# Performance work log

Hardware: AMD Instinct MI355X
Metric: run time of the kernel (lower is better)

The kernel has to match this reference:

```python
import jax, jax.numpy as jnp
import numpy as np

B, S, D = 8, 2048, 2048
E, R, K = 8, 16, 2
NUM_TASKS, NUM_MODES = 4, 2
ALPHA = 16.0


def setup_inputs() -> dict:
    key = jax.random.key(0)
    k1, k2, k3, k4 = jax.random.split(key, 4)
    hidden_states = jax.random.normal(k1, (B, S, D), dtype=jnp.float32)
    gate_w = jax.random.normal(k2, (E, D), dtype=jnp.float32) * 0.01  # nn.init.normal_(std=0.01)
    # Soft-prior biases: fill(-1.0), strong prior 3.0 / 2.0 at configured (task, expert) / (mode, expert)
    tb = -np.ones((NUM_TASKS, E), dtype=np.float32)
    mb = -np.ones((NUM_MODES, E), dtype=np.float32)
    for e in range(E):
        tb[e % NUM_TASKS, e] = 3.0
        mb[e % NUM_MODES, e] = 2.0
    # LoRA params; lora_B is zero-init in torch but we use small random values for a nontrivial baseline
    lora_A = jax.random.normal(k3, (E, R, D), dtype=jnp.float32) * (1.0 / np.sqrt(D))
    lora_B = jax.random.normal(k4, (E, D, R), dtype=jnp.float32) * 0.02
    return {
        "hidden_states": hidden_states,
        "gate_w": gate_w,
        "task_bias": jnp.asarray(tb),
        "mode_bias": jnp.asarray(mb),
        "lora_A": lora_A,
        "lora_B": lora_B,
        "task_id": 1,
        "mode_id": 1,
    }


def reference(hidden_states, gate_w, task_bias, mode_bias, lora_A, lora_B, task_id, mode_id):
    scaling = ALPHA / R
    # Router: score = dynamic_gate(mean_pool(x)) + task_bias[t] + mode_bias[m]
    x_pooled = hidden_states.mean(axis=1)                       # [B, D]
    logits = x_pooled @ gate_w.T + task_bias[task_id] + mode_bias[mode_id]  # [B, E]
    top_v, top_i = jax.lax.top_k(logits, K)                     # [B, K]
    weights = jax.nn.softmax(top_v, axis=-1)                    # [B, K]
    # per-sample, per-expert combine weight: sum of top-k weights routed to that expert
    one_hot = jax.nn.one_hot(top_i, E, dtype=weights.dtype)     # [B, K, E]
    sw = jnp.einsum('bke,bk->be', one_hot, weights)             # [B, E]
    # LoRA experts: (x @ A_e^T) @ B_e^T * scaling, weighted-summed per sample
    mid = jnp.einsum('bsd,erd->besr', hidden_states, lora_A)    # [B, E, S, R] (small: R=16)
    out = jnp.einsum('be,besr,edr->bsd', sw, mid, lora_B) * scaling  # [B, S, D]
    return out
```

## Files before the change

### kernel.cpp

```cpp
#include <hip/hip_runtime.h>
#include <stdint.h>

typedef __attribute__((ext_vector_type(8))) short bf16x8;
typedef __attribute__((ext_vector_type(4))) float f32x4;
typedef unsigned short ushort_t;

#define B_ 8
#define S_ 2048
#define D_ 2048
#define E_ 8
#define J_ 128

static __device__ __forceinline__ unsigned short f2bf(float f) {
  union { float f; uint32_t u; } v; v.f = f;
  uint32_t u = v.u;
  return (unsigned short)((u + 0x7FFFu + ((u >> 16) & 1u)) >> 16);
}
static __device__ __forceinline__ float bf2f(ushort_t h) {
  union { uint32_t u; float f; } v; v.u = ((uint32_t)h) << 16;
  return v.f;
}

#define GLL16(gsrc, ldst)                                                        \
  __builtin_amdgcn_global_load_lds(                                              \
      (const __attribute__((address_space(1))) void*)(gsrc),                     \
      (__attribute__((address_space(3))) void*)(ldst), 16, 0, 0)

#define VMBAR(N)                                                                 \
  asm volatile("s_waitcnt vmcnt(" #N ") lgkmcnt(0)\n\ts_barrier" ::: "memory")

__global__ void k_prep(const float* __restrict__ lA, const float* __restrict__ lB,
                       ushort_t* __restrict__ Ag, ushort_t* __restrict__ Bg) {
  int gid = blockIdx.x * blockDim.x + threadIdx.x;
  int stride = gridDim.x * blockDim.x;
  for (int o = gid; o < 32 * 128 * 8 * 8; o += stride) {
    int wi = o & 7, ch = o >> 3;
    int kt = ch >> 10, i = ch & 1023;
    int j = i >> 3, c = i & 7;
    int d = kt * 64 + (((c ^ j) & 7) << 3) + wi;
    Ag[o] = f2bf(lA[j * D_ + d]);
  }
  for (int o4 = gid; o4 < (D_ * J_) / 4; o4 += stride) {
    int j4 = o4 & 31, dd = o4 >> 5;
    int e = j4 >> 2, r0 = (j4 & 3) * 4;
    float4 v = *(const float4*)(lB + ((size_t)e * D_ + dd) * 16 + r0);
    uint2 pk;
    pk.x = (uint32_t)f2bf(v.x) | ((uint32_t)f2bf(v.y) << 16);
    pk.y = (uint32_t)f2bf(v.z) | ((uint32_t)f2bf(v.w) << 16);
    ((uint2*)Bg)[o4] = pk;
  }
}

__global__ __launch_bounds__(256) void k_mid(const float* __restrict__ x,
    const ushort_t* __restrict__ Ag, const float* __restrict__ gw,
    ushort_t* __restrict__ midb, float* __restrict__ lpart) {
  __shared__ float Xs[3][2048];
  __shared__ ushort_t Ab[2][8192];
  __shared__ float poolL[2048];
  __shared__ float tmpP[2][4][64];
  const int tid = threadIdx.x;
  const int w = tid >> 6, lane = tid & 63;
  const int lm = lane & 15, g = lane >> 4;
  const int b = blockIdx.y, s0 = blockIdx.x * 32;
  const int row16 = (w & 1) * 16, jbase = (w >> 1) * 64;
  const float* xb = x + ((size_t)(b * S_ + s0)) * D_;

  f32x4 acc[4] = {};

  auto stageX = [&](int buf, int kt) {
    const int d0 = kt * 64;
#pragma unroll
    for (int c = 0; c < 2; ++c) {
      int i = c * 256 + w * 64 + lane;
      int row = i >> 4, ch = i & 15;
      const float* src = xb + (size_t)row * D_ + d0 + ((ch ^ (row & 7)) << 2);
      GLL16(src, &Xs[buf][(c * 256 + w * 64) * 4]);
    }
  };
  auto stageA = [&](int buf, int kt) {
#pragma unroll
    for (int c = 0; c < 4; ++c) {
      const ushort_t* src = Ag + (size_t)kt * 8192 + (size_t)(c * 256 + w * 64 + lane) * 8;
      GLL16(src, &Ab[buf][(c * 256 + w * 64) * 8]);
    }
  };
  auto computeTile = [&](int t, int xcb, int acb) {
    const int r = row16 + lm;
#pragma unroll
    for (int ks = 0; ks < 2; ++ks) {
      const int c0 = ks * 8 + g * 2;
      float4 v0 = *(const float4*)&Xs[xcb][r * 64 + ((c0 ^ (r & 7)) << 2)];
      float4 v1 = *(const float4*)&Xs[xcb][r * 64 + (((c0 + 1) ^ (r & 7)) << 2)];
      bf16x8 xf;
      xf[0] = (short)f2bf(v0.x); xf[1] = (short)f2bf(v0.y);
      xf[2] = (short)f2bf(v0.z); xf[3] = (short)f2bf(v0.w);
      xf[4] = (short)f2bf(v1.x); xf[5] = (short)f2bf(v1.y);
      xf[6] = (short)f2bf(v1.z); xf[7] = (short)f2bf(v1.w);
#pragma unroll
      for (int nn = 0; nn < 4; ++nn) {
        int jr = jbase + nn * 16 + lm;
        bf16x8 af = *(const bf16x8*)&Ab[acb][jr * 64 + (((ks * 4 + g) ^ (jr & 7)) << 3)];
        acc[nn] = __builtin_amdgcn_mfma_f32_16x16x32_bf16(af, xf, acc[nn], 0, 0, 0);
      }
    }
    float s = 0.f;
#pragma unroll
    for (int i = 0; i < 8; ++i) {
      int rr = w * 8 + i;
      s += Xs[xcb][rr * 64 + (((lane >> 2) ^ (rr & 7)) << 2) + (lane & 3)];
    }
    tmpP[t & 1][w][lane] = s;
  };
  auto foldTile = [&](int tau) {
    if (w == (tau & 3)) {
      float cs = tmpP[tau & 1][0][lane] + tmpP[tau & 1][1][lane] +
                 tmpP[tau & 1][2][lane] + tmpP[tau & 1][3][lane];
      poolL[tau * 64 + lane] = cs;
    }
  };

  stageA(0, 0);
  __builtin_amdgcn_sched_barrier(0);
  stageX(0, 0);
  __builtin_amdgcn_sched_barrier(0);
  stageX(1, 1);
  __builtin_amdgcn_sched_barrier(0);

  int xcb = 0, xsb = 2;
  for (int t = 0; t < 31; ++t) {
    VMBAR(2);
    __builtin_amdgcn_sched_barrier(0);
    const int acb = t & 1;
    stageA(acb ^ 1, t + 1);
    __builtin_amdgcn_sched_barrier(0);
    if (t + 2 < 32) stageX(xsb, t + 2);
    __builtin_amdgcn_sched_barrier(0);
    if (t > 0) foldTile(t - 1);
    computeTile(t, xcb, acb);
    xcb = (xcb == 2) ? 0 : xcb + 1;
    xsb = (xsb == 2) ? 0 : xsb + 1;
  }
  VMBAR(0);
  __builtin_amdgcn_sched_barrier(0);
  foldTile(30);
  computeTile(31, xcb, 1);

  ushort_t* mp = midb + ((size_t)(b * S_ + s0 + row16 + lm)) * J_ + jbase;
#pragma unroll
  for (int nn = 0; nn < 4; ++nn) {
    uint2 pk;
    pk.x = (uint32_t)f2bf(acc[nn][0]) | ((uint32_t)f2bf(acc[nn][1]) << 16);
    pk.y = (uint32_t)f2bf(acc[nn][2]) | ((uint32_t)f2bf(acc[nn][3]) << 16);
    *(uint2*)&mp[nn * 16 + g * 4] = pk;
  }

  __syncthreads();
  foldTile(31);
  __syncthreads();

  float lp[8] = {0.f, 0.f, 0.f, 0.f, 0.f, 0.f, 0.f, 0.f};
#pragma unroll
  for (int k = 0; k < 8; ++k) {
    float pv = poolL[k * 256 + tid];
#pragma unroll
    for (int e = 0; e < 8; ++e) lp[e] += pv * gw[(size_t)e * D_ + k * 256 + tid];
  }
#pragma unroll
  for (int e = 0; e < 8; ++e) {
    float v = lp[e];
    v += __shfl_xor(v, 32); v += __shfl_xor(v, 16); v += __shfl_xor(v, 8);
    v += __shfl_xor(v, 4);  v += __shfl_xor(v, 2);  v += __shfl_xor(v, 1);
    if (lane == 0) tmpP[0][w][e] = v;
  }
  __syncthreads();
  if (tid < 8) {
    float s = tmpP[0][0][tid] + tmpP[0][1][tid] + tmpP[0][2][tid] + tmpP[0][3][tid];
    lpart[((size_t)(b * 64 + blockIdx.x)) * 8 + tid] = s;
  }
}

__global__ void k_router(const float* __restrict__ lpart,
                         const float* __restrict__ tb, const float* __restrict__ mb,
                         const int* __restrict__ task_p, const int* __restrict__ mode_p,
                         float* __restrict__ rinfo) {
  __shared__ float lg[64];
  const int t = threadIdx.x;
  const int b = t >> 3, e = t & 7;
  float s = 0.f;
  for (int k = 0; k < 64; ++k) s += lpart[((size_t)(b * 64 + k)) * 8 + e];
  lg[t] = s * (1.f / (float)S_) + tb[task_p[0] * E_ + e] + mb[mode_p[0] * E_ + e];
  __syncthreads();
  if (t < B_) {
    float v[8];
#pragma unroll
    for (int e2 = 0; e2 < 8; ++e2) v[e2] = lg[t * 8 + e2];
    int i1 = 0;
#pragma unroll
    for (int e2 = 1; e2 < 8; ++e2) if (v[e2] > v[i1]) i1 = e2;
    int i2 = (i1 == 0) ? 1 : 0;
#pragma unroll
    for (int e2 = 0; e2 < 8; ++e2) if (e2 != i1 && v[e2] > v[i2]) i2 = e2;
    float ex = __expf(v[i2] - v[i1]);
    float w1 = 1.f / (1.f + ex), w2 = ex * w1;
    float4 r;
    r.x = (float)i1; r.y = (float)i2; r.z = w1; r.w = w2;
    ((float4*)rinfo)[t] = r;
  }
}

__global__ __launch_bounds__(256) void k_comb(const ushort_t* __restrict__ midb,
    const float* __restrict__ rinfo, const ushort_t* __restrict__ Bg,
    float* __restrict__ out) {
  __shared__ ushort_t Bt[128][40];
  const int n = blockIdx.x, m = blockIdx.y, b = blockIdx.z;
  const int tid = threadIdx.x, w = tid >> 6, lane = tid & 63;
  const int lm = lane & 15, g = lane >> 4;

  const float4 ri = ((const float4*)rinfo)[b];
  const int i1 = (int)ri.x, i2 = (int)ri.y;
  const float w1 = ri.z, w2 = ri.w;

#pragma unroll
  for (int c = 0; c < 2; ++c) {
    int ci = c * 256 + tid;
    int d = ci >> 2, sub = ci & 3;
    int e = (sub & 2) ? i2 : i1;
    float sc = (sub & 2) ? w2 : w1;
    bf16x8 bv = *(const bf16x8*)(Bg + ((size_t)(n * 128 + d)) * J_ + e * 16 + (sub & 1) * 8);
    bf16x8 bw;
#pragma unroll
    for (int i = 0; i < 8; ++i) bw[i] = (short)f2bf(bf2f((ushort_t)bv[i]) * sc);
    *(bf16x8*)&Bt[d][sub * 8] = bw;
  }

  const int srow = m * 64 + w * 16 + lm;
  const int jw = (g < 2) ? (i1 * 16 + g * 8) : (i2 * 16 + (g - 2) * 8);
  bf16x8 pf = *(const bf16x8*)&midb[((size_t)(b * S_ + srow)) * J_ + jw];
  __syncthreads();

  f32x4 acc[8] = {};
#pragma unroll
  for (int nn = 0; nn < 8; ++nn) {
    bf16x8 af = *(const bf16x8*)&Bt[nn * 16 + lm][g * 8];
    acc[nn] = __builtin_amdgcn_mfma_f32_16x16x32_bf16(af, pf, acc[nn], 0, 0, 0);
  }

  float* op = out + ((size_t)(b * S_ + srow)) * D_ + n * 128;
#pragma unroll
  for (int nn = 0; nn < 8; ++nn)
    *(f32x4*)&op[nn * 16 + g * 4] = acc[nn];
}

extern "C" void kernel_launch(void* const* d_in, const int* in_sizes, int n_in,
                              void* d_out, int out_size, void* d_ws, size_t ws_size,
                              hipStream_t stream) {
  const float* x    = (const float*)d_in[0];
  const float* gw   = (const float*)d_in[1];
  const float* tb   = (const float*)d_in[2];
  const float* mb   = (const float*)d_in[3];
  const float* lA   = (const float*)d_in[4];
  const float* lB   = (const float*)d_in[5];
  const int* task_p = (const int*)d_in[6];
  const int* mode_p = (const int*)d_in[7];
  float* out = (float*)d_out;
  char* ws = (char*)d_ws;
  ushort_t* midb  = (ushort_t*)ws;
  ushort_t* Ag    = (ushort_t*)(ws + 4194304);
  ushort_t* Bg    = (ushort_t*)(ws + 4718592);
  float* lpart    = (float*)(ws + 5242880);
  float* rinfo    = (float*)(ws + 5259264);

  hipLaunchKernelGGL(k_prep, dim3(256), dim3(256), 0, stream, lA, lB, Ag, Bg);
  hipLaunchKernelGGL(k_mid, dim3(64, 8), dim3(256), 0, stream, x, Ag, gw, midb, lpart);
  hipLaunchKernelGGL(k_router, dim3(1), dim3(64), 0, stream,
                     lpart, tb, mb, task_p, mode_p, rinfo);
  hipLaunchKernelGGL(k_comb, dim3(16, 32, 8), dim3(256), 0, stream, midb, rinfo, Bg, out);
}
```

Baseline: 88.78 us.

## Fold router gate into LoRA-A MFMA and load x directly into registers

The gate weights are appended as extra rows (padded to 160) to the bf16 LoRA-A tile, so the router logits come out of the same MFMA pass as mid instead of a separate mean-pool and fp32 gate dot product in the kernel tail. The x tile is now read from global memory straight into registers with double buffering instead of being staged through LDS, which frees shared memory and removes the LDS pooling reductions. The gate projection is now done with bf16 x and gate weights rather than fp32, which can perturb logits and top-k routing. Wave 3 also does extra MFMA work, so the waves are unbalanced.

```diff
diff --git a/kernel.cpp b/kernel.cpp
--- a/kernel.cpp
+++ b/kernel.cpp
@@ -10,6 +10,8 @@
 #define D_ 2048
 #define E_ 8
 #define J_ 128
+#define AROWS 160
+#define ATILE (AROWS * 64)
 
 static __device__ __forceinline__ unsigned short f2bf(float f) {
   union { float f; uint32_t u; } v; v.f = f;
@@ -27,18 +29,30 @@
       (__attribute__((address_space(3))) void*)(ldst), 16, 0, 0)
 
 #define VMBAR(N)                                                                 \
-  asm volatile("s_waitcnt vmcnt(" #N ") lgkmcnt(0)\n\ts_barrier" ::: "memory")
+  asm volatile("s_waitcnt vmcnt(" #N ")\n\ts_barrier" ::: "memory")
 
 __global__ void k_prep(const float* __restrict__ lA, const float* __restrict__ lB,
-                       ushort_t* __restrict__ Ag, ushort_t* __restrict__ Bg) {
+                       const float* __restrict__ gw,
+                       ushort_t* __restrict__ AgE, ushort_t* __restrict__ Bg) {
   int gid = blockIdx.x * blockDim.x + threadIdx.x;
   int stride = gridDim.x * blockDim.x;
-  for (int o = gid; o < 32 * 128 * 8 * 8; o += stride) {
-    int wi = o & 7, ch = o >> 3;
-    int kt = ch >> 10, i = ch & 1023;
-    int j = i >> 3, c = i & 7;
-    int d = kt * 64 + (((c ^ j) & 7) << 3) + wi;
-    Ag[o] = f2bf(lA[j * D_ + d]);
+  for (int o = gid; o < 32 * AROWS * 8; o += stride) {
+    int kt = o / (AROWS * 8);
+    int rem = o - kt * (AROWS * 8);
+    int row = rem >> 3, c = rem & 7;
+    int d = kt * 64 + (((c ^ row) & 7) << 3);
+    bf16x8 outv = {};
+    if (row < 136) {
+      const float* src = (row < 128) ? (lA + (size_t)row * D_ + d)
+                                     : (gw + (size_t)(row - 128) * D_ + d);
+      float4 v0 = *(const float4*)src;
+      float4 v1 = *(const float4*)(src + 4);
+      outv[0] = (short)f2bf(v0.x); outv[1] = (short)f2bf(v0.y);
+      outv[2] = (short)f2bf(v0.z); outv[3] = (short)f2bf(v0.w);
+      outv[4] = (short)f2bf(v1.x); outv[5] = (short)f2bf(v1.y);
+      outv[6] = (short)f2bf(v1.z); outv[7] = (short)f2bf(v1.w);
+    }
+    *(bf16x8*)&AgE[(size_t)o * 8] = outv;
   }
   for (int o4 = gid; o4 < (D_ * J_) / 4; o4 += stride) {
     int j4 = o4 & 31, dd = o4 >> 5;
@@ -52,130 +66,123 @@
 }
 
 __global__ __launch_bounds__(256) void k_mid(const float* __restrict__ x,
-    const ushort_t* __restrict__ Ag, const float* __restrict__ gw,
-    ushort_t* __restrict__ midb, float* __restrict__ lpart) {
-  __shared__ float Xs[3][2048];
-  __shared__ ushort_t Ab[2][8192];
-  __shared__ float poolL[2048];
-  __shared__ float tmpP[2][4][64];
+    const ushort_t* __restrict__ AgE, ushort_t* __restrict__ midb,
+    float* __restrict__ lpart) {
+  __shared__ ushort_t Ab[2][ATILE];
   const int tid = threadIdx.x;
   const int w = tid >> 6, lane = tid & 63;
   const int lm = lane & 15, g = lane >> 4;
   const int b = blockIdx.y, s0 = blockIdx.x * 32;
-  const int row16 = (w & 1) * 16, jbase = (w >> 1) * 64;
-  const float* xb = x + ((size_t)(b * S_ + s0)) * D_;
-
-  f32x4 acc[4] = {};
-
-  auto stageX = [&](int buf, int kt) {
-    const int d0 = kt * 64;
-#pragma unroll
-    for (int c = 0; c < 2; ++c) {
-      int i = c * 256 + w * 64 + lane;
-      int row = i >> 4, ch = i & 15;
-      const float* src = xb + (size_t)row * D_ + d0 + ((ch ^ (row & 7)) << 2);
-      GLL16(src, &Xs[buf][(c * 256 + w * 64) * 4]);
-    }
-  };
+  const int tn0 = w, tn1 = w + 4;
+  const float* xrow = x + ((size_t)(b * S_ + s0 + lm)) * D_ + g * 8;
+
+  f32x4 acc0[2] = {}, acc1[2] = {}, acc2[2] = {};
+
   auto stageA = [&](int buf, int kt) {
 #pragma unroll
-    for (int c = 0; c < 4; ++c) {
-      const ushort_t* src = Ag + (size_t)kt * 8192 + (size_t)(c * 256 + w * 64 + lane) * 8;
-      GLL16(src, &Ab[buf][(c * 256 + w * 64) * 8]);
-    }
-  };
-  auto computeTile = [&](int t, int xcb, int acb) {
-    const int r = row16 + lm;
+    for (int c = 0; c < 5; ++c) {
+      int ch = c * 256 + tid;
+      const ushort_t* src = AgE + (size_t)kt * ATILE + (size_t)ch * 8;
+      GLL16(src, &Ab[buf][ch * 8]);
+    }
+  };
+  auto loadX = [&](float4* xr, int t) {
+    const float* p0 = xrow + t * 64;
+    const float* p1 = p0 + 16 * D_;
+    xr[0] = *(const float4*)(p0);
+    xr[1] = *(const float4*)(p0 + 4);
+    xr[2] = *(const float4*)(p0 + 32);
+    xr[3] = *(const float4*)(p0 + 36);
+    xr[4] = *(const float4*)(p1);
+    xr[5] = *(const float4*)(p1 + 4);
+    xr[6] = *(const float4*)(p1 + 32);
+    xr[7] = *(const float4*)(p1 + 36);
+  };
+  auto computeTile = [&](int t, const float4* xr) {
+    const ushort_t* Ac = &Ab[t & 1][0];
+    bf16x8 xf[2][2];
+#pragma unroll
+    for (int sh = 0; sh < 2; ++sh)
+#pragma unroll
+      for (int ks = 0; ks < 2; ++ks) {
+        float4 v0 = xr[sh * 4 + ks * 2];
+        float4 v1 = xr[sh * 4 + ks * 2 + 1];
+        bf16x8 f;
+        f[0] = (short)f2bf(v0.x); f[1] = (short)f2bf(v0.y);
+        f[2] = (short)f2bf(v0.z); f[3] = (short)f2bf(v0.w);
+        f[4] = (short)f2bf(v1.x); f[5] = (short)f2bf(v1.y);
+        f[6] = (short)f2bf(v1.z); f[7] = (short)f2bf(v1.w);
+        xf[sh][ks] = f;
+      }
 #pragma unroll
     for (int ks = 0; ks < 2; ++ks) {
-      const int c0 = ks * 8 + g * 2;
-      float4 v0 = *(const float4*)&Xs[xcb][r * 64 + ((c0 ^ (r & 7)) << 2)];
-      float4 v1 = *(const float4*)&Xs[xcb][r * 64 + (((c0 + 1) ^ (r & 7)) << 2)];
-      bf16x8 xf;
-      xf[0] = (short)f2bf(v0.x); xf[1] = (short)f2bf(v0.y);
-      xf[2] = (short)f2bf(v0.z); xf[3] = (short)f2bf(v0.w);
-      xf[4] = (short)f2bf(v1.x); xf[5] = (short)f2bf(v1.y);
-      xf[6] = (short)f2bf(v1.z); xf[7] = (short)f2bf(v1.w);
-#pragma unroll
-      for (int nn = 0; nn < 4; ++nn) {
-        int jr = jbase + nn * 16 + lm;
-        bf16x8 af = *(const bf16x8*)&Ab[acb][jr * 64 + (((ks * 4 + g) ^ (jr & 7)) << 3)];
-        acc[nn] = __builtin_amdgcn_mfma_f32_16x16x32_bf16(af, xf, acc[nn], 0, 0, 0);
+      const int chs = (((ks * 4 + g) ^ (lm & 7)) << 3);
+      bf16x8 a0 = *(const bf16x8*)&Ac[(tn0 * 16 + lm) * 64 + chs];
+      bf16x8 a1 = *(const bf16x8*)&Ac[(tn1 * 16 + lm) * 64 + chs];
+#pragma unroll
+      for (int sh = 0; sh < 2; ++sh) {
+        acc0[sh] = __builtin_amdgcn_mfma_f32_16x16x32_bf16(a0, xf[sh][ks], acc0[sh], 0, 0, 0);
+        acc1[sh] = __builtin_amdgcn_mfma_f32_16x16x32_bf16(a1, xf[sh][ks], acc1[sh], 0, 0, 0);
       }
-    }
-    float s = 0.f;
-#pragma unroll
-    for (int i = 0; i < 8; ++i) {
-      int rr = w * 8 + i;
-      s += Xs[xcb][rr * 64 + (((lane >> 2) ^ (rr & 7)) << 2) + (lane & 3)];
-    }
-    tmpP[t & 1][w][lane] = s;
-  };
-  auto foldTile = [&](int tau) {
-    if (w == (tau & 3)) {
-      float cs = tmpP[tau & 1][0][lane] + tmpP[tau & 1][1][lane] +
-                 tmpP[tau & 1][2][lane] + tmpP[tau & 1][3][lane];
-      poolL[tau * 64 + lane] = cs;
-    }
-  };
-
+      if (w == 3) {
+        bf16x8 a2 = *(const bf16x8*)&Ac[(128 + lm) * 64 + chs];
+#pragma unroll
+        for (int sh = 0; sh < 2; ++sh)
+          acc2[sh] = __builtin_amdgcn_mfma_f32_16x16x32_bf16(a2, xf[sh][ks], acc2[sh], 0, 0, 0);
+      }
+    }
+  };
+
+  float4 xA[8], xB[8];
   stageA(0, 0);
   __builtin_amdgcn_sched_barrier(0);
-  stageX(0, 0);
+  loadX(xA, 0);
   __builtin_amdgcn_sched_barrier(0);
-  stageX(1, 1);
+
+  auto body = [&](int t, const float4* xc, float4* xn) {
+    VMBAR(8);
+    __builtin_amdgcn_sched_barrier(0);
+    stageA((t + 1) & 1, t + 1);
+    __builtin_amdgcn_sched_barrier(0);
+    loadX(xn, t + 1);
+    __builtin_amdgcn_sched_barrier(0);
+    computeTile(t, xc);
+  };
+
+  for (int tt = 0; tt < 15; ++tt) {
+    body(2 * tt, xA, xB);
+    body(2 * tt + 1, xB, xA);
+  }
+  body(30, xA, xB);
+  VMBAR(8);
   __builtin_amdgcn_sched_barrier(0);
-
-  int xcb = 0, xsb = 2;
-  for (int t = 0; t < 31; ++t) {
-    VMBAR(2);
-    __builtin_amdgcn_sched_barrier(0);
-    const int acb = t & 1;
-    stageA(acb ^ 1, t + 1);
-    __builtin_amdgcn_sched_barrier(0);
-    if (t + 2 < 32) stageX(xsb, t + 2);
-    __builtin_amdgcn_sched_barrier(0);
-    if (t > 0) foldTile(t - 1);
-    computeTile(t, xcb, acb);
-    xcb = (xcb == 2) ? 0 : xcb + 1;
-    xsb = (xsb == 2) ? 0 : xsb + 1;
-  }
-  VMBAR(0);
-  __builtin_amdgcn_sched_barrier(0);
-  foldTile(30);
-  computeTile(31, xcb, 1);
-
-  ushort_t* mp = midb + ((size_t)(b * S_ + s0 + row16 + lm)) * J_ + jbase;
-#pragma unroll
-  for (int nn = 0; nn < 4; ++nn) {
-    uint2 pk;
-    pk.x = (uint32_t)f2bf(acc[nn][0]) | ((uint32_t)f2bf(acc[nn][1]) << 16);
-    pk.y = (uint32_t)f2bf(acc[nn][2]) | ((uint32_t)f2bf(acc[nn][3]) << 16);
-    *(uint2*)&mp[nn * 16 + g * 4] = pk;
-  }
-
-  __syncthreads();
-  foldTile(31);
-  __syncthreads();
-
-  float lp[8] = {0.f, 0.f, 0.f, 0.f, 0.f, 0.f, 0.f, 0.f};
-#pragma unroll
-  for (int k = 0; k < 8; ++k) {
-    float pv = poolL[k * 256 + tid];
-#pragma unroll
-    for (int e = 0; e < 8; ++e) lp[e] += pv * gw[(size_t)e * D_ + k * 256 + tid];
-  }
-#pragma unroll
-  for (int e = 0; e < 8; ++e) {
-    float v = lp[e];
-    v += __shfl_xor(v, 32); v += __shfl_xor(v, 16); v += __shfl_xor(v, 8);
-    v += __shfl_xor(v, 4);  v += __shfl_xor(v, 2);  v += __shfl_xor(v, 1);
-    if (lane == 0) tmpP[0][w][e] = v;
-  }
-  __syncthreads();
-  if (tid < 8) {
-    float s = tmpP[0][0][tid] + tmpP[0][1][tid] + tmpP[0][2][tid] + tmpP[0][3][tid];
-    lpart[((size_t)(b * 64 + blockIdx.x)) * 8 + tid] = s;
+  computeTile(31, xB);
+
+#pragma unroll
+  for (int sh = 0; sh < 2; ++sh) {
+    ushort_t* mp = midb + ((size_t)(b * S_ + s0 + sh * 16 + lm)) * J_;
+    uint2 pk0, pk1;
+    pk0.x = (uint32_t)f2bf(acc0[sh][0]) | ((uint32_t)f2bf(acc0[sh][1]) << 16);
+    pk0.y = (uint32_t)f2bf(acc0[sh][2]) | ((uint32_t)f2bf(acc0[sh][3]) << 16);
+    pk1.x = (uint32_t)f2bf(acc1[sh][0]) | ((uint32_t)f2bf(acc1[sh][1]) << 16);
+    pk1.y = (uint32_t)f2bf(acc1[sh][2]) | ((uint32_t)f2bf(acc1[sh][3]) << 16);
+    *(uint2*)&mp[tn0 * 16 + g * 4] = pk0;
+    *(uint2*)&mp[tn1 * 16 + g * 4] = pk1;
+  }
+
+  if (w == 3) {
+    float lsum[4];
+#pragma unroll
+    for (int q = 0; q < 4; ++q) {
+      float v = acc2[0][q] + acc2[1][q];
+      v += __shfl_xor(v, 1); v += __shfl_xor(v, 2);
+      v += __shfl_xor(v, 4); v += __shfl_xor(v, 8);
+      lsum[q] = v;
+    }
+    if (lm == 0 && g < 2) {
+      float* lp = lpart + ((size_t)(b * 64 + blockIdx.x)) * 8 + g * 4;
+      lp[0] = lsum[0]; lp[1] = lsum[1]; lp[2] = lsum[2]; lp[3] = lsum[3];
+    }
   }
 }
 
@@ -264,14 +271,14 @@
   const int* mode_p = (const int*)d_in[7];
   float* out = (float*)d_out;
   char* ws = (char*)d_ws;
-  ushort_t* midb  = (ushort_t*)ws;
-  ushort_t* Ag    = (ushort_t*)(ws + 4194304);
-  ushort_t* Bg    = (ushort_t*)(ws + 4718592);
-  float* lpart    = (float*)(ws + 5242880);
-  float* rinfo    = (float*)(ws + 5259264);
-
-  hipLaunchKernelGGL(k_prep, dim3(256), dim3(256), 0, stream, lA, lB, Ag, Bg);
-  hipLaunchKernelGGL(k_mid, dim3(64, 8), dim3(256), 0, stream, x, Ag, gw, midb, lpart);
+  ushort_t* midb = (ushort_t*)ws;
+  ushort_t* AgE  = (ushort_t*)(ws + 4194304);
+  ushort_t* Bg   = (ushort_t*)(ws + 4849664);
+  float* lpart   = (float*)(ws + 5373952);
+  float* rinfo   = (float*)(ws + 5390336);
+
+  hipLaunchKernelGGL(k_prep, dim3(256), dim3(256), 0, stream, lA, lB, gw, AgE, Bg);
+  hipLaunchKernelGGL(k_mid, dim3(64, 8), dim3(256), 0, stream, x, AgE, midb, lpart);
   hipLaunchKernelGGL(k_router, dim3(1), dim3(64), 0, stream,
                      lpart, tb, mb, task_p, mode_p, rinfo);
   hipLaunchKernelGGL(k_comb, dim3(16, 32, 8), dim3(256), 0, stream, midb, rinfo, Bg, out);
```

After: 122.1 us. +37.5%, slower.
